# Optimization experiments

Measured on AMD Instinct MI355X. Metric: run time of the kernel, lower is better.

The kernel has to match this reference:

```python
import jax, jax.numpy as jnp
import numpy as np

NUM_LAYERS = 3
N = 4096
DIM = 512
TOPK = 8
BIG = 1.0e9
EPS_COS = 1e-8
EPS_NORM = 1e-12
BN_EPS = 1e-5
LAM_K = 64.0
LAM_Z = 16.0
SIGMA_INTRA = 0.99
ALPHA = np.linspace(1.0, 1.2, NUM_LAYERS)
BETA = np.linspace(0.0, 0.0, NUM_LAYERS)


def setup_inputs() -> dict:
    key = jax.random.key(0)
    ks = jax.random.split(key, 6)
    feats = jax.random.normal(ks[0], (NUM_LAYERS, N, DIM), dtype=jnp.float32)
    labels = jax.random.randint(ks[1], (N,), 0, 64, dtype=jnp.int64)
    fc1_w = jax.random.normal(ks[2], (NUM_LAYERS, DIM, DIM), dtype=jnp.float32) * (1.0 / np.sqrt(DIM))
    fc2_w = jax.random.normal(ks[3], (NUM_LAYERS, DIM, DIM), dtype=jnp.float32) * (1.0 / np.sqrt(DIM))
    bn_gamma = jnp.ones((NUM_LAYERS, DIM), dtype=jnp.float32)
    bn_beta = jnp.zeros((NUM_LAYERS, DIM), dtype=jnp.float32)
    proj_w = jax.random.normal(ks[4], (768, DIM), dtype=jnp.float32) * (1.0 / np.sqrt(DIM))
    return {"feats": feats, "labels": labels, "fc1_w": fc1_w, "fc2_w": fc2_w,
            "bn_gamma": bn_gamma, "bn_beta": bn_beta, "proj_w": proj_w}


def _l2norm(x, axis=-1):
    return x / jnp.maximum(jnp.linalg.norm(x, axis=axis, keepdims=True), EPS_NORM)


def _pairwise_cosine(G):
    Gn = _l2norm(G)
    sim = Gn @ Gn.T
    return jnp.clip(sim, -1.0 + EPS_COS, 1.0 - EPS_COS)


def _knn_mask(sim, base_mask, topk):
    n = sim.shape[0]
    masked = (sim - BIG * jnp.eye(n, dtype=sim.dtype)) * base_mask - (1.0 - base_mask) * BIG
    k = min(topk, max(n - 1, 1))
    idx = jax.lax.top_k(masked, k)[1]  # [N, k]
    st = jnp.zeros_like(sim).at[jnp.arange(n)[:, None], idx].set(1.0)
    return jnp.maximum(st, st.T)


def _build_intra_inter(sim, labels, topk):
    same = (labels[None, :] == labels[:, None]).astype(sim.dtype)
    diff = 1.0 - same
    m_intra = _knn_mask(sim, same, topk)
    m_inter = _knn_mask(sim, diff, topk)
    sim_intra = jnp.maximum(sim * m_intra, 0.0)
    sim_inter = jnp.maximum(sim * m_inter, 0.0)
    return sim_intra, sim_inter


def _normalize_sym(sim_graph, eps=1e-8):
    d = jnp.maximum(sim_graph.sum(axis=1), eps)
    dinv = d ** -0.5
    return dinv[:, None] * sim_graph * dinv[None, :]  # == diag(dinv) @ S @ diag(dinv)


def _diffusion(K, t_diff=1):
    out = K
    for _ in range(max(t_diff - 1, 0)):
        out = out @ K
    return out


def _bn_train(x, gamma, beta):
    m = x.mean(axis=0)
    v = x.var(axis=0)  # biased, as torch BN training
    return (x - m) / jnp.sqrt(v + BN_EPS) * gamma + beta


def _gam(S, G, w1, w2, gamma, beta):
    Z = S @ (G @ w1.T)
    Z = jax.nn.relu(_bn_train(Z, gamma, beta))
    Z = S @ (Z @ w2.T)
    return Z + G


def reference(feats, labels, fc1_w, fc2_w, bn_gamma, bn_beta, proj_w):
    n = feats.shape[1]
    eye = jnp.eye(n, dtype=feats.dtype)
    same = (labels[None, :] == labels[:, None]).astype(feats.dtype)

    K_list, Z_list = [], []
    for i in range(NUM_LAYERS):
        G = feats[i]
        sim = _pairwise_cosine(G)
        sim_intra, sim_inter = _build_intra_inter(sim, labels, TOPK)
        sim_graph = float(ALPHA[i]) * sim_intra + float(BETA[i]) * sim_inter + 1e-6 * eye
        S = _normalize_sym(sim_graph)
        K = _diffusion(S, t_diff=1)
        Z = _gam(S, G, fc1_w[i], fc2_w[i], bn_gamma[i], bn_beta[i])
        K_list.append(K)
        Z_list.append(Z)

    loss_K = jnp.zeros((), dtype=feats.dtype)
    loss_Z = jnp.zeros((), dtype=feats.dtype)
    for i in range(1, NUM_LAYERS):
        K_tgt = jax.lax.stop_gradient(K_list[i])
        loss_K = loss_K + jnp.mean((K_list[i - 1] - K_tgt) ** 2)
        Zp = _l2norm(Z_list[i - 1] @ proj_w.T)
        Zc = _l2norm(Z_list[i] @ proj_w.T)
        loss_Z = loss_Z + jnp.mean((Zp - jax.lax.stop_gradient(Zc)) ** 2)

    K_idea = _diffusion(same * SIGMA_INTRA, t_diff=1)
    loss_idea = jnp.mean((K_list[-1] - K_idea) ** 2)
    return LAM_K * loss_K + LAM_Z * loss_Z + loss_idea
```

## Files before the change

kernel.cpp:

```cpp
#include <hip/hip_runtime.h>
#include <math.h>
#include <stdint.h>

#define NROWS 4096
#define DIM   512
#define NCLS  64
#define CAP   128
#define PD    768
#define NL    3

typedef __attribute__((ext_vector_type(8))) short short8v;
typedef __attribute__((ext_vector_type(4))) float f32x4;

__device__ __forceinline__ unsigned short f2bf(float f) {
  unsigned u = __float_as_uint(f);
  unsigned r = (u + 0x7FFF + ((u >> 16) & 1)) >> 16;
  return (unsigned short)r;
}

__device__ __forceinline__ void gload_lds16(const void* g, void* l) {
  auto* lp = reinterpret_cast<__attribute__((address_space(3))) unsigned int*>(
      reinterpret_cast<uintptr_t>(l));
  const auto* gp = reinterpret_cast<const __attribute__((address_space(1))) unsigned int*>(
      reinterpret_cast<uintptr_t>(g));
  __builtin_amdgcn_global_load_lds(gp, lp, 16, 0, 0);
}

__device__ __forceinline__ float waveReduce(float v) {
#pragma unroll
  for (int o = 32; o > 0; o >>= 1) v += __shfl_down(v, o);
  return v;
}

__device__ __forceinline__ float blockReduce(float v) {
  __shared__ float sh[4];
  int lane = threadIdx.x & 63, wv = threadIdx.x >> 6;
  v = waveReduce(v);
  if (lane == 0) sh[wv] = v;
  __syncthreads();
  float t = 0.f;
  if (threadIdx.x == 0) {
    int nw = (blockDim.x + 63) >> 6;
    for (int i = 0; i < nw; ++i) t += sh[i];
  }
  return t;
}

__global__ __launch_bounds__(256) void k_hist(const int* __restrict__ labels, int* __restrict__ chunkCnt) {
  __shared__ int h[NCLS];
  int t = threadIdx.x;
  if (t < NCLS) h[t] = 0;
  __syncthreads();
  atomicAdd(&h[labels[blockIdx.x * 256 + t]], 1);
  __syncthreads();
  if (t < NCLS) chunkCnt[blockIdx.x * NCLS + t] = h[t];
}

__global__ void k_scan(const int* __restrict__ chunkCnt, int* __restrict__ cnt,
                       int* __restrict__ off, int* __restrict__ chunkBase, float* __restrict__ acc) {
  __shared__ int sc[NCLS];
  int c = threadIdx.x;
  if (c < 8) acc[c] = 0.f;
  int tot = 0;
  for (int b = 0; b < 16; ++b) tot += chunkCnt[b * NCLS + c];
  cnt[c] = tot;
  sc[c] = tot;
  __syncthreads();
  if (c == 0) {
    int s = 0;
    for (int i = 0; i < NCLS; ++i) { int tv = sc[i]; sc[i] = s; s += tv; }
  }
  __syncthreads();
  int run = sc[c];
  off[c] = run;
  for (int b = 0; b < 16; ++b) { chunkBase[b * NCLS + c] = run; run += chunkCnt[b * NCLS + c]; }
  if (c == 0) off[NCLS] = NROWS;
}

__global__ __launch_bounds__(256) void k_scatter(const int* __restrict__ labels, const int* __restrict__ chunkBase,
                                                 int* __restrict__ perm, int* __restrict__ clsp) {
  __shared__ int lab[256];
  int t = threadIdx.x;
  int r = blockIdx.x * 256 + t;
  int c = labels[r];
  lab[t] = c;
  __syncthreads();
  int rank = 0;
  for (int j = 0; j < t; ++j) rank += (lab[j] == c);
  int pos = chunkBase[blockIdx.x * NCLS + c] + rank;
  perm[pos] = r;
  clsp[pos] = c;
}

__global__ __launch_bounds__(128) void k_prep(const float* __restrict__ feats, const int* __restrict__ perm,
                                              unsigned short* __restrict__ Gpb, float* __restrict__ invn) {
  __shared__ float red[2];
  int l = blockIdx.y;
  const float* G = feats + (size_t)l * NROWS * DIM;
  unsigned short* Gp = Gpb + (size_t)l * NROWS * DIM;
  int row = blockIdx.x, t = threadIdx.x;
  const float4* src = (const float4*)(G + (size_t)perm[row] * DIM);
  float4 v = src[t];
  ushort4 b;
  b.x = f2bf(v.x); b.y = f2bf(v.y); b.z = f2bf(v.z); b.w = f2bf(v.w);
  *(ushort4*)(Gp + (size_t)row * DIM + t * 4) = b;
  float ss = v.x * v.x + v.y * v.y + v.z * v.z + v.w * v.w;
  ss = waveReduce(ss);
  if ((t & 63) == 0) red[t >> 6] = ss;
  __syncthreads();
  if (t == 0) invn[l * NROWS + row] = 1.f / fmaxf(sqrtf(red[0] + red[1]), 1e-12f);
}

__global__ __launch_bounds__(256) void k_tobf16all(const float4* __restrict__ fc1, const float4* __restrict__ fc2,
                                                   const float4* __restrict__ proj,
                                                   ushort4* __restrict__ w1, ushort4* __restrict__ w2,
                                                   ushort4* __restrict__ pj) {
  const int nW = NL * DIM * DIM / 4;
  const int nP = PD * DIM / 4;
  int i = blockIdx.x * 256 + threadIdx.x;
  const float4* src; ushort4* dst; int k;
  if (i < nW) { src = fc1; dst = w1; k = i; }
  else if (i < 2 * nW) { src = fc2; dst = w2; k = i - nW; }
  else if (i < 2 * nW + nP) { src = proj; dst = pj; k = i - 2 * nW; }
  else return;
  float4 v = src[k];
  ushort4 o;
  o.x = f2bf(v.x); o.y = f2bf(v.y); o.z = f2bf(v.z); o.w = f2bf(v.w);
  dst[k] = o;
}

__global__ __launch_bounds__(256) void k_sim(const unsigned short* __restrict__ Gpb,
                                             const float* __restrict__ invn,
                                             const int* __restrict__ cnt, const int* __restrict__ off,
                                             float* __restrict__ sim) {
  int l = blockIdx.z;
  const unsigned short* Gp = Gpb + (size_t)l * NROWS * DIM;
  const float* inv = invn + (size_t)l * NROWS;
  float* sm = sim + (size_t)l * NCLS * CAP * CAP;
  int c = blockIdx.y;
  int n = min(cnt[c], CAP);
  int ti = blockIdx.x >> 2, tj = blockIdx.x & 3;
  if (ti * 32 >= n || tj * 32 >= n) return;
  int base = off[c];
  __shared__ short As[32][40];
  __shared__ short Bs[32][40];
  const int t = threadIdx.x;
  const int lane = t & 63, wv = t >> 6;
  const int qi = wv >> 1, qj = wv & 1;
  const int fr = lane & 15, kg = lane >> 4;
  const int half = t >> 7, tt = t & 127;
  const int srow = tt >> 2, scol = (tt & 3) * 8;
  int gr = (half ? tj : ti) * 32 + srow;
  const unsigned short* ps = Gp + (size_t)(base + min(gr, n - 1)) * DIM + scol;
  short* dst = half ? &Bs[srow][scol] : &As[srow][scol];
  f32x4 acc = {};
  for (int k0 = 0; k0 < DIM; k0 += 32) {
    short8v v = *(const short8v*)(ps + k0);
    __syncthreads();
    *(short8v*)dst = v;
    __syncthreads();
    short8v af = *(const short8v*)&As[qi * 16 + fr][kg * 8];
    short8v bf = *(const short8v*)&Bs[qj * 16 + fr][kg * 8];
    acc = __builtin_amdgcn_mfma_f32_16x16x32_bf16(af, bf, acc, 0, 0, 0);
  }
  int gj = tj * 32 + qj * 16 + fr;
  int r0 = ti * 32 + qi * 16 + kg * 4;
  if (gj < n) {
    float sj = inv[base + gj];
#pragma unroll
    for (int r = 0; r < 4; ++r) {
      int gi = r0 + r;
      if (gi < n) {
        float v = acc[r] * inv[base + gi] * sj;
        v = fminf(fmaxf(v, -1.0f + 1e-8f), 1.0f - 1e-8f);
        sm[((size_t)c * CAP + gi) * CAP + gj] = v;
      }
    }
  }
}

__global__ __launch_bounds__(256) void k_topk(const float* __restrict__ sim, const int* __restrict__ cnt,
                                              const int* __restrict__ off, const int* __restrict__ clsp,
                                              int* __restrict__ t8) {
  int l = blockIdx.y;
  const float* sm = sim + (size_t)l * NCLS * CAP * CAP;
  int* t8l = t8 + (size_t)l * NROWS * 8;
  int pr = blockIdx.x * 256 + threadIdx.x;
  if (pr >= NROWS) return;
  int c = clsp[pr];
  int n = min(cnt[c], CAP);
  int loc = pr - off[c];
  const float4* row4 = (const float4*)(sm + ((size_t)c * CAP + loc) * CAP);
  float bv[8]; int bi[8];
#pragma unroll
  for (int q = 0; q < 8; ++q) { bv[q] = -3e38f; bi[q] = -1; }
  for (int j4 = 0; j4 < CAP / 4; ++j4) {
    if (j4 * 4 >= n) break;
    float4 v4 = row4[j4];
    float vv[4] = {v4.x, v4.y, v4.z, v4.w};
#pragma unroll
    for (int k = 0; k < 4; ++k) {
      int j = j4 * 4 + k;
      if (j >= n || j == loc) continue;
      float v = vv[k];
      if (v > bv[7]) {
        bv[7] = v; bi[7] = j;
#pragma unroll
        for (int q = 7; q > 0; --q) {
          if (bv[q] > bv[q - 1]) {
            float tv = bv[q]; bv[q] = bv[q - 1]; bv[q - 1] = tv;
            int tq = bi[q]; bi[q] = bi[q - 1]; bi[q - 1] = tq;
          }
        }
      }
    }
  }
#pragma unroll
  for (int q = 0; q < 8; ++q) t8l[pr * 8 + q] = bi[q];
}

__global__ __launch_bounds__(256) void k_buildS1(const float* __restrict__ sim, const int* __restrict__ cnt,
                                                 const int* __restrict__ off, const int* __restrict__ t8,
                                                 float* __restrict__ S, float* __restrict__ dinv) {
  int l = blockIdx.z;
  float alpha = 1.0f + 0.1f * l;
  const float* sm = sim + (size_t)l * NCLS * CAP * CAP;
  float* Sl = S + (size_t)l * NCLS * CAP * CAP;
  const int* t8l = t8 + (size_t)l * NROWS * 8;
  float* dv = dinv + (size_t)l * NCLS * CAP;
  int c = blockIdx.x;
  int n = min(cnt[c], CAP);
  int i0 = blockIdx.y * 32;
  if (i0 >= n) return;
  int base = off[c];
  __shared__ int sh8[CAP * 8];
  for (int i = threadIdx.x; i < n * 8; i += 256) sh8[i] = t8l[base * 8 + i];
  __syncthreads();
  int r = threadIdx.x >> 3;
  int lj = threadIdx.x & 7;
  int i = i0 + r;
  float d = 0.f;
  if (i < n) {
    int my8[8];
#pragma unroll
    for (int q = 0; q < 8; ++q) my8[q] = sh8[i * 8 + q];
    const float* srow = sm + ((size_t)c * CAP + i) * CAP;
    float* wrow = Sl + ((size_t)c * CAP + i) * CAP;
    for (int j = lj; j < n; j += 8) {
      float w;
      if (j == i) w = 1e-6f;
      else {
        bool m = false;
#pragma unroll
        for (int q = 0; q < 8; ++q) m = m || (my8[q] == j) || (sh8[j * 8 + q] == i);
        w = m ? alpha * fmaxf(srow[j], 0.f) : 0.f;
      }
      wrow[j] = w;
      d += w;
    }
  }
  d += __shfl_xor(d, 1);
  d += __shfl_xor(d, 2);
  d += __shfl_xor(d, 4);
  if (lj == 0 && i < n) dv[c * CAP + i] = 1.f / sqrtf(fmaxf(d, 1e-8f));
}

__global__ __launch_bounds__(256) void k_buildS2(float* __restrict__ S, const float* __restrict__ dinv,
                                                 const int* __restrict__ cnt) {
  int l = blockIdx.z;
  float* Sl = S + (size_t)l * NCLS * CAP * CAP;
  const float* dv = dinv + (size_t)l * NCLS * CAP;
  int c = blockIdx.x;
  int n = min(cnt[c], CAP);
  int i0 = blockIdx.y * 32;
  if (i0 >= n) return;
  __shared__ float sd[CAP];
  for (int k = threadIdx.x; k < n; k += 256) sd[k] = dv[c * CAP + k];
  __syncthreads();
  for (int p = threadIdx.x; p < 32 * CAP; p += 256) {
    int r = p >> 7, j = p & (CAP - 1);
    int i = i0 + r;
    if (i < n && j < n)
      Sl[((size_t)c * CAP + i) * CAP + j] *= sd[i] * sd[j];
  }
}

__global__ __launch_bounds__(256) void k_gemm_bf16(const short* __restrict__ A, const short* __restrict__ B,
                                                   float* __restrict__ C, unsigned short* __restrict__ Cb,
                                                   int N, long sA, long sB, long sC) {
  int l = blockIdx.z;
  A += (size_t)l * sA; B += (size_t)l * sB;
  if (Cb) Cb += (size_t)l * sC; else C += (size_t)l * sC;
  __shared__ __align__(16) short As[128][32];
  __shared__ __align__(16) short Bs[128][32];
  const int row0 = blockIdx.x * 128, col0 = blockIdx.y * 128;
  const int t = threadIdx.x;
  const int lane = t & 63, wv = t >> 6;
  const int wm = wv >> 1, wn = wv & 1;
  const int fr = lane & 15, kg = lane >> 4;
  const int srow = lane >> 2, skb = (lane & 3) * 8;
  const short* pa = A + (size_t)(row0 + wv * 32 + srow) * DIM + skb;
  const short* pb = B + (size_t)(col0 + wv * 32 + srow) * DIM + skb;
  f32x4 acc[4][4] = {};
  for (int kt = 0; kt < DIM; kt += 32) {
    __syncthreads();
    gload_lds16(pa + kt, &As[wv * 32][0]);
    gload_lds16(pa + kt + (size_t)16 * DIM, &As[wv * 32 + 16][0]);
    gload_lds16(pb + kt, &Bs[wv * 32][0]);
    gload_lds16(pb + kt + (size_t)16 * DIM, &Bs[wv * 32 + 16][0]);
    __syncthreads();
    short8v af[4], bf[4];
#pragma unroll
    for (int i = 0; i < 4; ++i) {
      af[i] = *(const short8v*)&As[wm * 64 + i * 16 + fr][kg * 8];
      bf[i] = *(const short8v*)&Bs[wn * 64 + i * 16 + fr][kg * 8];
    }
#pragma unroll
    for (int i = 0; i < 4; ++i)
#pragma unroll
      for (int j = 0; j < 4; ++j)
        acc[i][j] = __builtin_amdgcn_mfma_f32_16x16x32_bf16(af[i], bf[j], acc[i][j], 0, 0, 0);
  }
#pragma unroll
  for (int i = 0; i < 4; ++i) {
    int r0 = row0 + wm * 64 + i * 16 + kg * 4;
#pragma unroll
    for (int j = 0; j < 4; ++j) {
      int cc = col0 + wn * 64 + j * 16 + fr;
#pragma unroll
      for (int r = 0; r < 4; ++r) {
        if (Cb) Cb[(size_t)(r0 + r) * N + cc] = f2bf(acc[i][j][r]);
        else C[(size_t)(r0 + r) * N + cc] = acc[i][j][r];
      }
    }
  }
}

__global__ __launch_bounds__(256) void k_spmm4(const float* __restrict__ S, const float* __restrict__ X,
                                               const float* __restrict__ Gfeat, const int* __restrict__ perm,
                                               float* __restrict__ Y, unsigned short* __restrict__ Yb,
                                               const int* __restrict__ cnt, const int* __restrict__ off) {
  int l = blockIdx.z >> 2;
  int zc = blockIdx.z & 3;
  const float* Sl = S + (size_t)l * NCLS * CAP * CAP;
  const float4* X4 = (const float4*)(X + (size_t)l * NROWS * DIM);
  const float4* G4 = Gfeat ? (const float4*)(Gfeat + (size_t)l * NROWS * DIM) : (const float4*)nullptr;
  float4* Y4 = Y ? (float4*)(Y + (size_t)l * NROWS * DIM) : (float4*)nullptr;
  ushort4* Yb4 = Yb ? (ushort4*)(Yb + (size_t)l * NROWS * DIM) : (ushort4*)nullptr;
  int c = blockIdx.x;
  int n = min(cnt[c], CAP);
  int i0 = zc * 32;
  if (i0 >= n) return;
  int base = off[c];
  int col4 = blockIdx.y * 64 + (threadIdx.x & 63);
  int ty = threadIdx.x >> 6;
  __shared__ float sS[32][CAP];
  for (int idx = threadIdx.x; idx < 32 * n; idx += 256) {
    int r = idx / n, j = idx - r * n;
    sS[r][j] = (i0 + r < n) ? Sl[((size_t)c * CAP + i0 + r) * CAP + j] : 0.f;
  }
  __syncthreads();
  float4 acc[8];
#pragma unroll
  for (int ii = 0; ii < 8; ++ii) acc[ii] = make_float4(0.f, 0.f, 0.f, 0.f);
#pragma unroll 4
  for (int j = 0; j < n; ++j) {
    float4 x = X4[(size_t)(base + j) * 128 + col4];
#pragma unroll
    for (int ii = 0; ii < 8; ++ii) {
      float s = sS[ty * 8 + ii][j];
      acc[ii].x += s * x.x;
      acc[ii].y += s * x.y;
      acc[ii].z += s * x.z;
      acc[ii].w += s * x.w;
    }
  }
#pragma unroll
  for (int ii = 0; ii < 8; ++ii) {
    int r = i0 + ty * 8 + ii;
    if (r < n) {
      size_t o = (size_t)(base + r) * 128 + col4;
      float4 v = acc[ii];
      if (G4) {
        float4 g = G4[(size_t)perm[base + r] * 128 + col4];
        v.x += g.x; v.y += g.y; v.z += g.z; v.w += g.w;
      }
      if (Yb4) {
        ushort4 ob;
        ob.x = f2bf(v.x); ob.y = f2bf(v.y); ob.z = f2bf(v.z); ob.w = f2bf(v.w);
        Yb4[o] = ob;
      } else {
        Y4[o] = v;
      }
    }
  }
}

#define PARTSZ (size_t)((NROWS / 32) * 1024)

__global__ __launch_bounds__(256) void k_colstats(const float* __restrict__ X, float* __restrict__ part) {
  int l = blockIdx.y;
  const float* Xl = X + (size_t)l * NROWS * DIM;
  float* pl = part + (size_t)l * PARTSZ;
  int rb = blockIdx.x, t = threadIdx.x;
#pragma unroll
  for (int cp = 0; cp < 2; ++cp) {
    int col = cp * 256 + t;
    float s = 0.f, s2 = 0.f;
    for (int r = 0; r < 32; ++r) {
      float v = Xl[(size_t)(rb * 32 + r) * DIM + col];
      s += v; s2 += v * v;
    }
    pl[rb * 1024 + col] = s;
    pl[rb * 1024 + 512 + col] = s2;
  }
}

__global__ __launch_bounds__(64) void k_bnfin(const float* __restrict__ part, const float* __restrict__ gamma,
                                              const float* __restrict__ beta, float* __restrict__ sc) {
  int l = blockIdx.y;
  const float* pl = part + (size_t)l * PARTSZ;
  int k = blockIdx.x * 64 + threadIdx.x;
  float s = 0.f, s2 = 0.f;
  for (int b = 0; b < NROWS / 32; ++b) {
    s += pl[b * 1024 + k];
    s2 += pl[b * 1024 + 512 + k];
  }
  float m = s * (1.f / NROWS);
  float var = s2 * (1.f / NROWS) - m * m;
  float sg = gamma[l * DIM + k] / sqrtf(var + 1e-5f);
  sc[l * 2 * DIM + k] = sg;
  sc[l * 2 * DIM + DIM + k] = beta[l * DIM + k] - m * sg;
}

__global__ __launch_bounds__(256) void k_bnrelu(const float4* __restrict__ X, const float* __restrict__ sc,
                                                ushort4* __restrict__ Yb) {
  int l = blockIdx.y;
  const float4* Xl = X + (size_t)l * (NROWS * DIM / 4);
  const float* scl = sc + (size_t)l * 2 * DIM;
  ushort4* Yl = Yb + (size_t)l * (NROWS * DIM / 4);
  int i = blockIdx.x * blockDim.x + threadIdx.x;
  int cb = (i * 4) & (DIM - 1);
  float4 v = Xl[i];
  ushort4 o;
  o.x = f2bf(fmaxf(v.x * scl[cb + 0] + scl[DIM + cb + 0], 0.f));
  o.y = f2bf(fmaxf(v.y * scl[cb + 1] + scl[DIM + cb + 1], 0.f));
  o.z = f2bf(fmaxf(v.z * scl[cb + 2] + scl[DIM + cb + 2], 0.f));
  o.w = f2bf(fmaxf(v.w * scl[cb + 3] + scl[DIM + cb + 3], 0.f));
  Yl[i] = o;
}

__global__ __launch_bounds__(192) void k_rownormP(float* __restrict__ P) {
  __shared__ float red[3];
  __shared__ float s_inv;
  int l = blockIdx.y;
  float* Pl = P + (size_t)l * NROWS * PD;
  int row = blockIdx.x, t = threadIdx.x;
  float4* p = (float4*)(Pl + (size_t)row * PD);
  float4 v = p[t];
  float ss = v.x * v.x + v.y * v.y + v.z * v.z + v.w * v.w;
  ss = waveReduce(ss);
  if ((t & 63) == 0) red[t >> 6] = ss;
  __syncthreads();
  if (t == 0) s_inv = 1.f / fmaxf(sqrtf(red[0] + red[1] + red[2]), 1e-12f);
  __syncthreads();
  float inv = s_inv;
  v.x *= inv; v.y *= inv; v.z *= inv; v.w *= inv;
  p[t] = v;
}

__global__ __launch_bounds__(256) void k_lossdiff(const float* __restrict__ P, int n, float coef,
                                                  float* __restrict__ acc) {
  int y = blockIdx.y;
  const float* A = P + (size_t)y * NROWS * PD;
  const float* B = A + (size_t)NROWS * PD;
  float s = 0.f;
  for (int i = blockIdx.x * blockDim.x + threadIdx.x; i < n; i += gridDim.x * blockDim.x) {
    float d = A[i] - B[i];
    s += d * d;
  }
  s = blockReduce(s);
  if (threadIdx.x == 0) atomicAdd(acc, s * coef);
}

__global__ __launch_bounds__(256) void k_lossS(const float* __restrict__ S, const int* __restrict__ cnt,
                                               float target, float cK, float cI,
                                               float* __restrict__ acc) {
  int y = blockIdx.y;
  const float* Sa = S + (size_t)y * NCLS * CAP * CAP;
  const float* Sb = nullptr;
  float coef;
  if (y < 2) { Sb = Sa + (size_t)NCLS * CAP * CAP; coef = cK; }
  else { Sa = S + (size_t)2 * NCLS * CAP * CAP; coef = cI; }
  int c = blockIdx.x;
  int n = min(cnt[c], CAP);
  float s = 0.f;
  for (int p = threadIdx.x; p < CAP * CAP; p += 256) {
    int i = p >> 7, j = p & (CAP - 1);
    if (i < n && j < n) {
      size_t o = ((size_t)c * CAP + i) * CAP + j;
      float d = Sb ? (Sa[o] - Sb[o]) : (Sa[o] - target);
      s += d * d;
    }
  }
  s = blockReduce(s);
  if (threadIdx.x == 0) atomicAdd(acc, s * coef);
}

__global__ void k_final(const float* __restrict__ acc, float* __restrict__ out) {
  if (threadIdx.x == 0) out[0] = acc[0];
}

extern "C" void kernel_launch(void* const* d_in, const int* in_sizes, int n_in,
                              void* d_out, int out_size, void* d_ws, size_t ws_size,
                              hipStream_t stream) {
  const float* feats = (const float*)d_in[0];
  const int* labels = (const int*)d_in[1];
  const float* fc1 = (const float*)d_in[2];
  const float* fc2 = (const float*)d_in[3];
  const float* gamma = (const float*)d_in[4];
  const float* beta = (const float*)d_in[5];
  const float* proj = (const float*)d_in[6];
  float* out = (float*)d_out;

  char* w = (char*)d_ws;
  auto alloc = [&](size_t bytes) { char* p = w; w += (bytes + 255) & ~(size_t)255; return p; };
  float* bufA = (float*)alloc((size_t)NL * NROWS * DIM * 4);
  float* bufB = (float*)alloc((size_t)NL * NROWS * DIM * 4);
  unsigned short* Gpb = (unsigned short*)alloc((size_t)NL * NROWS * DIM * 2);
  unsigned short* actb = (unsigned short*)alloc((size_t)NL * NROWS * DIM * 2);
  unsigned short* W1b = (unsigned short*)alloc((size_t)NL * DIM * DIM * 2);
  unsigned short* W2b = (unsigned short*)alloc((size_t)NL * DIM * DIM * 2);
  unsigned short* Pjb = (unsigned short*)alloc((size_t)PD * DIM * 2);
  float* sim  = (float*)alloc((size_t)NL * NCLS * CAP * CAP * 4);
  float* S    = (float*)alloc((size_t)NL * NCLS * CAP * CAP * 4);
  float* P    = (float*)alloc((size_t)NL * NROWS * PD * 4);
  float* invn = (float*)alloc((size_t)NL * NROWS * 4);
  float* dinv = (float*)alloc((size_t)NL * NCLS * CAP * 4);
  float* part = (float*)alloc((size_t)NL * PARTSZ * 4);
  float* bnsc = (float*)alloc((size_t)NL * 2 * DIM * 4);
  float* acc  = (float*)alloc(256);
  int* cnt  = (int*)alloc(NCLS * 4);
  int* offc = (int*)alloc((NCLS + 1) * 4);
  int* perm = (int*)alloc(NROWS * 4);
  int* clsp = (int*)alloc(NROWS * 4);
  int* t8   = (int*)alloc((size_t)NL * NROWS * 8 * 4);
  int* chunkCnt  = (int*)alloc(16 * NCLS * 4);
  int* chunkBase = (int*)alloc(16 * NCLS * 4);

  const float LAM_K = 64.f, LAM_Z = 16.f, SIGMA = 0.99f;
  const float cK = LAM_K / ((float)NROWS * (float)NROWS);
  const float cZ = LAM_Z / ((float)NROWS * (float)PD);
  const float cI = 1.f / ((float)NROWS * (float)NROWS);
  const long sAct = (long)NROWS * DIM;
  const long sW = (long)DIM * DIM;

  hipLaunchKernelGGL(k_hist, dim3(16), dim3(256), 0, stream, labels, chunkCnt);
  hipLaunchKernelGGL(k_scan, dim3(1), dim3(64), 0, stream, chunkCnt, cnt, offc, chunkBase, acc);
  hipLaunchKernelGGL(k_scatter, dim3(16), dim3(256), 0, stream, labels, chunkBase, perm, clsp);
  hipLaunchKernelGGL(k_tobf16all, dim3((2 * NL * DIM * DIM / 4 + PD * DIM / 4 + 255) / 256), dim3(256), 0, stream,
                     (const float4*)fc1, (const float4*)fc2, (const float4*)proj,
                     (ushort4*)W1b, (ushort4*)W2b, (ushort4*)Pjb);

  hipLaunchKernelGGL(k_prep, dim3(NROWS, NL), dim3(128), 0, stream, feats, perm, Gpb, invn);
  hipLaunchKernelGGL(k_sim, dim3(16, NCLS, NL), dim3(256), 0, stream, Gpb, invn, cnt, offc, sim);
  hipLaunchKernelGGL(k_topk, dim3(NROWS / 256, NL), dim3(256), 0, stream, sim, cnt, offc, clsp, t8);
  hipLaunchKernelGGL(k_buildS1, dim3(NCLS, CAP / 32, NL), dim3(256), 0, stream, sim, cnt, offc, t8, S, dinv);
  hipLaunchKernelGGL(k_buildS2, dim3(NCLS, CAP / 32, NL), dim3(256), 0, stream, S, dinv, cnt);

  hipLaunchKernelGGL(k_gemm_bf16, dim3(NROWS / 128, DIM / 128, NL), dim3(256), 0, stream,
                     (const short*)Gpb, (const short*)W1b, bufA, (unsigned short*)nullptr, DIM, sAct, sW, (long)NROWS * DIM);
  hipLaunchKernelGGL(k_spmm4, dim3(NCLS, DIM / 256, 4 * NL), dim3(256), 0, stream, S, bufA,
                     (const float*)nullptr, (const int*)nullptr, bufB, (unsigned short*)nullptr, cnt, offc);
  hipLaunchKernelGGL(k_colstats, dim3(NROWS / 32, NL), dim3(256), 0, stream, bufB, part);
  hipLaunchKernelGGL(k_bnfin, dim3(DIM / 64, NL), dim3(64), 0, stream, part, gamma, beta, bnsc);
  hipLaunchKernelGGL(k_bnrelu, dim3(NROWS * DIM / 4 / 256, NL), dim3(256), 0, stream,
                     (const float4*)bufB, bnsc, (ushort4*)actb);
  hipLaunchKernelGGL(k_gemm_bf16, dim3(NROWS / 128, DIM / 128, NL), dim3(256), 0, stream,
                     (const short*)actb, (const short*)W2b, bufB, (unsigned short*)nullptr, DIM, sAct, sW, (long)NROWS * DIM);
  hipLaunchKernelGGL(k_spmm4, dim3(NCLS, DIM / 256, 4 * NL), dim3(256), 0, stream, S, bufB,
                     feats, perm, (float*)nullptr, actb, cnt, offc);
  hipLaunchKernelGGL(k_gemm_bf16, dim3(NROWS / 128, PD / 128, NL), dim3(256), 0, stream,
                     (const short*)actb, (const short*)Pjb, P, (unsigned short*)nullptr, PD, sAct, 0L, (long)NROWS * PD);
  hipLaunchKernelGGL(k_rownormP, dim3(NROWS, NL), dim3(192), 0, stream, P);

  hipLaunchKernelGGL(k_lossS, dim3(NCLS, 3), dim3(256), 0, stream, S, cnt, SIGMA, cK, cI, acc);
  hipLaunchKernelGGL(k_lossdiff, dim3(512, 2), dim3(256), 0, stream, P, NROWS * PD, cZ, acc);

  hipLaunchKernelGGL(k_final, dim3(1), dim3(64), 0, stream, acc, out);
}
```

Before: 287.7 us.

## Fuse weight conversion, BN column stats, and loss kernels; shrink GEMM tiles

Folds the weight-to-bf16 conversion into the feature prep kernel as an extra grid row, computes BatchNorm column sums and sums of squares inside the first spmm epilogue instead of in a separate colstats pass, and merges the two loss kernels into one launch. It also changes the bf16 GEMM tile from 128x128 to 128x64, which gives more blocks for better occupancy at the cost of less reuse per block. The aim is to cut launch count and one full read of the activation buffer. The risk is extra shared-memory syncs in spmm and lower arithmetic intensity in the GEMM.

Result: faster. 265.2 us (-7.8%).

```diff
diff --git a/kernel.cpp b/kernel.cpp
--- a/kernel.cpp
+++ b/kernel.cpp
@@ -8,6 +8,7 @@
 #define CAP   128
 #define PD    768
 #define NL    3
+#define PARTSZ (size_t)(NCLS * 4 * 1024)
 
 typedef __attribute__((ext_vector_type(8))) short short8v;
 typedef __attribute__((ext_vector_type(4))) float f32x4;
@@ -92,10 +93,30 @@
   clsp[pos] = c;
 }
 
-__global__ __launch_bounds__(128) void k_prep(const float* __restrict__ feats, const int* __restrict__ perm,
-                                              unsigned short* __restrict__ Gpb, float* __restrict__ invn) {
+__global__ __launch_bounds__(128) void k_prepw(const float* __restrict__ feats, const int* __restrict__ perm,
+                                               unsigned short* __restrict__ Gpb, float* __restrict__ invn,
+                                               const float4* __restrict__ fc1, const float4* __restrict__ fc2,
+                                               const float4* __restrict__ proj,
+                                               ushort4* __restrict__ w1, ushort4* __restrict__ w2,
+                                               ushort4* __restrict__ pj) {
+  int y = blockIdx.y;
+  if (y == NL) {
+    const int nW = NL * DIM * DIM / 4;
+    const int nP = PD * DIM / 4;
+    int idx = blockIdx.x * 128 + threadIdx.x;
+    const float4* src; ushort4* dst; int k;
+    if (idx < nW) { src = fc1; dst = w1; k = idx; }
+    else if (idx < 2 * nW) { src = fc2; dst = w2; k = idx - nW; }
+    else if (idx < 2 * nW + nP) { src = proj; dst = pj; k = idx - 2 * nW; }
+    else return;
+    float4 v = src[k];
+    ushort4 o;
+    o.x = f2bf(v.x); o.y = f2bf(v.y); o.z = f2bf(v.z); o.w = f2bf(v.w);
+    dst[k] = o;
+    return;
+  }
   __shared__ float red[2];
-  int l = blockIdx.y;
+  int l = y;
   const float* G = feats + (size_t)l * NROWS * DIM;
   unsigned short* Gp = Gpb + (size_t)l * NROWS * DIM;
   int row = blockIdx.x, t = threadIdx.x;
@@ -109,24 +130,6 @@
   if ((t & 63) == 0) red[t >> 6] = ss;
   __syncthreads();
   if (t == 0) invn[l * NROWS + row] = 1.f / fmaxf(sqrtf(red[0] + red[1]), 1e-12f);
-}
-
-__global__ __launch_bounds__(256) void k_tobf16all(const float4* __restrict__ fc1, const float4* __restrict__ fc2,
-                                                   const float4* __restrict__ proj,
-                                                   ushort4* __restrict__ w1, ushort4* __restrict__ w2,
-                                                   ushort4* __restrict__ pj) {
-  const int nW = NL * DIM * DIM / 4;
-  const int nP = PD * DIM / 4;
-  int i = blockIdx.x * 256 + threadIdx.x;
-  const float4* src; ushort4* dst; int k;
-  if (i < nW) { src = fc1; dst = w1; k = i; }
-  else if (i < 2 * nW) { src = fc2; dst = w2; k = i - nW; }
-  else if (i < 2 * nW + nP) { src = proj; dst = pj; k = i - 2 * nW; }
-  else return;
-  float4 v = src[k];
-  ushort4 o;
-  o.x = f2bf(v.x); o.y = f2bf(v.y); o.z = f2bf(v.z); o.w = f2bf(v.w);
-  dst[k] = o;
 }
 
 __global__ __launch_bounds__(256) void k_sim(const unsigned short* __restrict__ Gpb,
@@ -286,52 +289,46 @@
 }
 
 __global__ __launch_bounds__(256) void k_gemm_bf16(const short* __restrict__ A, const short* __restrict__ B,
-                                                   float* __restrict__ C, unsigned short* __restrict__ Cb,
-                                                   int N, long sA, long sB, long sC) {
+                                                   float* __restrict__ C, int N,
+                                                   long sA, long sB, long sC) {
   int l = blockIdx.z;
-  A += (size_t)l * sA; B += (size_t)l * sB;
-  if (Cb) Cb += (size_t)l * sC; else C += (size_t)l * sC;
+  A += (size_t)l * sA; B += (size_t)l * sB; C += (size_t)l * sC;
   __shared__ __align__(16) short As[128][32];
-  __shared__ __align__(16) short Bs[128][32];
-  const int row0 = blockIdx.x * 128, col0 = blockIdx.y * 128;
+  __shared__ __align__(16) short Bs[64][32];
+  const int row0 = blockIdx.x * 128, col0 = blockIdx.y * 64;
   const int t = threadIdx.x;
   const int lane = t & 63, wv = t >> 6;
-  const int wm = wv >> 1, wn = wv & 1;
   const int fr = lane & 15, kg = lane >> 4;
   const int srow = lane >> 2, skb = (lane & 3) * 8;
   const short* pa = A + (size_t)(row0 + wv * 32 + srow) * DIM + skb;
-  const short* pb = B + (size_t)(col0 + wv * 32 + srow) * DIM + skb;
-  f32x4 acc[4][4] = {};
+  const short* pb = B + (size_t)(col0 + wv * 16 + srow) * DIM + skb;
+  f32x4 acc[2][4] = {};
   for (int kt = 0; kt < DIM; kt += 32) {
     __syncthreads();
     gload_lds16(pa + kt, &As[wv * 32][0]);
     gload_lds16(pa + kt + (size_t)16 * DIM, &As[wv * 32 + 16][0]);
-    gload_lds16(pb + kt, &Bs[wv * 32][0]);
-    gload_lds16(pb + kt + (size_t)16 * DIM, &Bs[wv * 32 + 16][0]);
+    gload_lds16(pb + kt, &Bs[wv * 16][0]);
     __syncthreads();
-    short8v af[4], bf[4];
-#pragma unroll
-    for (int i = 0; i < 4; ++i) {
-      af[i] = *(const short8v*)&As[wm * 64 + i * 16 + fr][kg * 8];
-      bf[i] = *(const short8v*)&Bs[wn * 64 + i * 16 + fr][kg * 8];
-    }
-#pragma unroll
-    for (int i = 0; i < 4; ++i)
+    short8v af[2], bf[4];
+#pragma unroll
+    for (int i = 0; i < 2; ++i) af[i] = *(const short8v*)&As[wv * 32 + i * 16 + fr][kg * 8];
+#pragma unroll
+    for (int j = 0; j < 4; ++j) bf[j] = *(const short8v*)&Bs[j * 16 + fr][kg * 8];
+#pragma unroll
+    for (int i = 0; i < 2; ++i)
 #pragma unroll
       for (int j = 0; j < 4; ++j)
         acc[i][j] = __builtin_amdgcn_mfma_f32_16x16x32_bf16(af[i], bf[j], acc[i][j], 0, 0, 0);
   }
 #pragma unroll
-  for (int i = 0; i < 4; ++i) {
-    int r0 = row0 + wm * 64 + i * 16 + kg * 4;
+  for (int i = 0; i < 2; ++i) {
+    int r0 = row0 + wv * 32 + i * 16 + kg * 4;
 #pragma unroll
     for (int j = 0; j < 4; ++j) {
-      int cc = col0 + wn * 64 + j * 16 + fr;
-#pragma unroll
-      for (int r = 0; r < 4; ++r) {
-        if (Cb) Cb[(size_t)(r0 + r) * N + cc] = f2bf(acc[i][j][r]);
-        else C[(size_t)(r0 + r) * N + cc] = acc[i][j][r];
-      }
+      int cc = col0 + j * 16 + fr;
+#pragma unroll
+      for (int r = 0; r < 4; ++r)
+        C[(size_t)(r0 + r) * N + cc] = acc[i][j][r];
     }
   }
 }
@@ -339,6 +336,7 @@
 __global__ __launch_bounds__(256) void k_spmm4(const float* __restrict__ S, const float* __restrict__ X,
                                                const float* __restrict__ Gfeat, const int* __restrict__ perm,
                                                float* __restrict__ Y, unsigned short* __restrict__ Yb,
+                                               float* __restrict__ part,
                                                const int* __restrict__ cnt, const int* __restrict__ off) {
   int l = blockIdx.z >> 2;
   int zc = blockIdx.z & 3;
@@ -350,11 +348,20 @@
   int c = blockIdx.x;
   int n = min(cnt[c], CAP);
   int i0 = zc * 32;
-  if (i0 >= n) return;
+  float* pslot = part ? part + (size_t)l * PARTSZ + (size_t)(c * 4 + zc) * 1024 : (float*)nullptr;
+  __shared__ float sS[32][CAP];
+  if (i0 >= n) {
+    if (pslot) {
+      int col = blockIdx.y * 256 + threadIdx.x;
+      pslot[col] = 0.f;
+      pslot[512 + col] = 0.f;
+    }
+    return;
+  }
   int base = off[c];
-  int col4 = blockIdx.y * 64 + (threadIdx.x & 63);
+  int lane = threadIdx.x & 63;
+  int col4 = blockIdx.y * 64 + lane;
   int ty = threadIdx.x >> 6;
-  __shared__ float sS[32][CAP];
   for (int idx = threadIdx.x; idx < 32 * n; idx += 256) {
     int r = idx / n, j = idx - r * n;
     sS[r][j] = (i0 + r < n) ? Sl[((size_t)c * CAP + i0 + r) * CAP + j] : 0.f;
@@ -363,7 +370,6 @@
   float4 acc[8];
 #pragma unroll
   for (int ii = 0; ii < 8; ++ii) acc[ii] = make_float4(0.f, 0.f, 0.f, 0.f);
-#pragma unroll 4
   for (int j = 0; j < n; ++j) {
     float4 x = X4[(size_t)(base + j) * 128 + col4];
 #pragma unroll
@@ -375,6 +381,7 @@
       acc[ii].w += s * x.w;
     }
   }
+  float s1[4] = {0.f, 0.f, 0.f, 0.f}, s2[4] = {0.f, 0.f, 0.f, 0.f};
 #pragma unroll
   for (int ii = 0; ii < 8; ++ii) {
     int r = i0 + ty * 8 + ii;
@@ -385,6 +392,10 @@
         float4 g = G4[(size_t)perm[base + r] * 128 + col4];
         v.x += g.x; v.y += g.y; v.z += g.z; v.w += g.w;
       }
+      if (pslot) {
+        s1[0] += v.x; s1[1] += v.y; s1[2] += v.z; s1[3] += v.w;
+        s2[0] += v.x * v.x; s2[1] += v.y * v.y; s2[2] += v.z * v.z; s2[3] += v.w * v.w;
+      }
       if (Yb4) {
         ushort4 ob;
         ob.x = f2bf(v.x); ob.y = f2bf(v.y); ob.z = f2bf(v.z); ob.w = f2bf(v.w);
@@ -394,25 +405,29 @@
       }
     }
   }
-}
-
-#define PARTSZ (size_t)((NROWS / 32) * 1024)
-
-__global__ __launch_bounds__(256) void k_colstats(const float* __restrict__ X, float* __restrict__ part) {
-  int l = blockIdx.y;
-  const float* Xl = X + (size_t)l * NROWS * DIM;
-  float* pl = part + (size_t)l * PARTSZ;
-  int rb = blockIdx.x, t = threadIdx.x;
-#pragma unroll
-  for (int cp = 0; cp < 2; ++cp) {
-    int col = cp * 256 + t;
-    float s = 0.f, s2 = 0.f;
-    for (int r = 0; r < 32; ++r) {
-      float v = Xl[(size_t)(rb * 32 + r) * DIM + col];
-      s += v; s2 += v * v;
-    }
-    pl[rb * 1024 + col] = s;
-    pl[rb * 1024 + 512 + col] = s2;
+  if (pslot) {
+    __syncthreads();
+    float* scr = &sS[0][0];
+#pragma unroll
+    for (int q = 0; q < 4; ++q) {
+      scr[(ty * 64 + lane) * 8 + q] = s1[q];
+      scr[(ty * 64 + lane) * 8 + 4 + q] = s2[q];
+    }
+    __syncthreads();
+    if (ty == 0) {
+#pragma unroll
+      for (int q = 0; q < 4; ++q) {
+        float a = 0.f, b = 0.f;
+#pragma unroll
+        for (int g = 0; g < 4; ++g) {
+          a += scr[(g * 64 + lane) * 8 + q];
+          b += scr[(g * 64 + lane) * 8 + 4 + q];
+        }
+        int col = blockIdx.y * 256 + lane * 4 + q;
+        pslot[col] = a;
+        pslot[512 + col] = b;
+      }
+    }
   }
 }
 
@@ -422,7 +437,7 @@
   const float* pl = part + (size_t)l * PARTSZ;
   int k = blockIdx.x * 64 + threadIdx.x;
   float s = 0.f, s2 = 0.f;
-  for (int b = 0; b < NROWS / 32; ++b) {
+  for (int b = 0; b < NCLS * 4; ++b) {
     s += pl[b * 1024 + k];
     s2 += pl[b * 1024 + 512 + k];
   }
@@ -469,42 +484,44 @@
   p[t] = v;
 }
 
-__global__ __launch_bounds__(256) void k_lossdiff(const float* __restrict__ P, int n, float coef,
-                                                  float* __restrict__ acc) {
+__global__ __launch_bounds__(256) void k_loss(const float* __restrict__ S, const float* __restrict__ P,
+                                              const int* __restrict__ cnt,
+                                              float target, float cK, float cI, float cZ,
+                                              float* __restrict__ acc) {
   int y = blockIdx.y;
-  const float* A = P + (size_t)y * NROWS * PD;
-  const float* B = A + (size_t)NROWS * PD;
-  float s = 0.f;
-  for (int i = blockIdx.x * blockDim.x + threadIdx.x; i < n; i += gridDim.x * blockDim.x) {
-    float d = A[i] - B[i];
-    s += d * d;
-  }
-  s = blockReduce(s);
-  if (threadIdx.x == 0) atomicAdd(acc, s * coef);
-}
-
-__global__ __launch_bounds__(256) void k_lossS(const float* __restrict__ S, const int* __restrict__ cnt,
-                                               float target, float cK, float cI,
-                                               float* __restrict__ acc) {
-  int y = blockIdx.y;
-  const float* Sa = S + (size_t)y * NCLS * CAP * CAP;
-  const float* Sb = nullptr;
-  float coef;
-  if (y < 2) { Sb = Sa + (size_t)NCLS * CAP * CAP; coef = cK; }
-  else { Sa = S + (size_t)2 * NCLS * CAP * CAP; coef = cI; }
-  int c = blockIdx.x;
-  int n = min(cnt[c], CAP);
-  float s = 0.f;
-  for (int p = threadIdx.x; p < CAP * CAP; p += 256) {
-    int i = p >> 7, j = p & (CAP - 1);
-    if (i < n && j < n) {
-      size_t o = ((size_t)c * CAP + i) * CAP + j;
-      float d = Sb ? (Sa[o] - Sb[o]) : (Sa[o] - target);
+  if (y < 3) {
+    if (blockIdx.x >= NCLS) return;
+    const float* Sa = S + (size_t)y * NCLS * CAP * CAP;
+    const float* Sb = nullptr;
+    float coef;
+    if (y < 2) { Sb = Sa + (size_t)NCLS * CAP * CAP; coef = cK; }
+    else { Sa = S + (size_t)2 * NCLS * CAP * CAP; coef = cI; }
+    int c = blockIdx.x;
+    int n = min(cnt[c], CAP);
+    float s = 0.f;
+    for (int p = threadIdx.x; p < CAP * CAP; p += 256) {
+      int i = p >> 7, j = p & (CAP - 1);
+      if (i < n && j < n) {
+        size_t o = ((size_t)c * CAP + i) * CAP + j;
+        float d = Sb ? (Sa[o] - Sb[o]) : (Sa[o] - target);
+        s += d * d;
+      }
+    }
+    s = blockReduce(s);
+    if (threadIdx.x == 0) atomicAdd(acc, s * coef);
+  } else {
+    int yy = y - 3;
+    const float* A = P + (size_t)yy * NROWS * PD;
+    const float* B = A + (size_t)NROWS * PD;
+    const int nel = NROWS * PD;
+    float s = 0.f;
+    for (int i = blockIdx.x * blockDim.x + threadIdx.x; i < nel; i += gridDim.x * blockDim.x) {
+      float d = A[i] - B[i];
       s += d * d;
     }
-  }
-  s = blockReduce(s);
-  if (threadIdx.x == 0) atomicAdd(acc, s * coef);
+    s = blockReduce(s);
+    if (threadIdx.x == 0) atomicAdd(acc, s * cZ);
+  }
 }
 
 __global__ void k_final(const float* __restrict__ acc, float* __restrict__ out) {
@@ -558,34 +575,32 @@
   hipLaunchKernelGGL(k_hist, dim3(16), dim3(256), 0, stream, labels, chunkCnt);
   hipLaunchKernelGGL(k_scan, dim3(1), dim3(64), 0, stream, chunkCnt, cnt, offc, chunkBase, acc);
   hipLaunchKernelGGL(k_scatter, dim3(16), dim3(256), 0, stream, labels, chunkBase, perm, clsp);
-  hipLaunchKernelGGL(k_tobf16all, dim3((2 * NL * DIM * DIM / 4 + PD * DIM / 4 + 255) / 256), dim3(256), 0, stream,
+
+  hipLaunchKernelGGL(k_prepw, dim3(NROWS, NL + 1), dim3(128), 0, stream, feats, perm, Gpb, invn,
                      (const float4*)fc1, (const float4*)fc2, (const float4*)proj,
                      (ushort4*)W1b, (ushort4*)W2b, (ushort4*)Pjb);
 
-  hipLaunchKernelGGL(k_prep, dim3(NROWS, NL), dim3(128), 0, stream, feats, perm, Gpb, invn);
   hipLaunchKernelGGL(k_sim, dim3(16, NCLS, NL), dim3(256), 0, stream, Gpb, invn, cnt, offc, sim);
   hipLaunchKernelGGL(k_topk, dim3(NROWS / 256, NL), dim3(256), 0, stream, sim, cnt, offc, clsp, t8);
   hipLaunchKernelGGL(k_buildS1, dim3(NCLS, CAP / 32, NL), dim3(256), 0, stream, sim, cnt, offc, t8, S, dinv);
   hipLaunchKernelGGL(k_buildS2, dim3(NCLS, CAP / 32, NL), dim3(256), 0, stream, S, dinv, cnt);
 
-  hipLaunchKernelGGL(k_gemm_bf16, dim3(NROWS / 128, DIM / 128, NL), dim3(256), 0, stream,
-                     (const short*)Gpb, (const short*)W1b, bufA, (unsigned short*)nullptr, DIM, sAct, sW, (long)NROWS * DIM);
+  hipLaunchKernelGGL(k_gemm_bf16, dim3(NROWS / 128, DIM / 64, NL), dim3(256), 0, stream,
+                     (const short*)Gpb, (const short*)W1b, bufA, DIM, sAct, sW, (long)NROWS * DIM);
   hipLaunchKernelGGL(k_spmm4, dim3(NCLS, DIM / 256, 4 * NL), dim3(256), 0, stream, S, bufA,
-                     (const float*)nullptr, (const int*)nullptr, bufB, (unsigned short*)nullptr, cnt, offc);
-  hipLaunchKernelGGL(k_colstats, dim3(NROWS / 32, NL), dim3(256), 0, stream, bufB, part);
+                     (const float*)nullptr, (const int*)nullptr, bufB, (unsigned short*)nullptr, part, cnt, offc);
   hipLaunchKernelGGL(k_bnfin, dim3(DIM / 64, NL), dim3(64), 0, stream, part, gamma, beta, bnsc);
   hipLaunchKernelGGL(k_bnrelu, dim3(NROWS * DIM / 4 / 256, NL), dim3(256), 0, stream,
                      (const float4*)bufB, bnsc, (ushort4*)actb);
-  hipLaunchKernelGGL(k_gemm_bf16, dim3(NROWS / 128, DIM / 128, NL), dim3(256), 0, stream,
-                     (const short*)actb, (const short*)W2b, bufB, (unsigned short*)nullptr, DIM, sAct, sW, (long)NROWS * DIM);
+  hipLaunchKernelGGL(k_gemm_bf16, dim3(NROWS / 128, DIM / 64, NL), dim3(256), 0, stream,
+                     (const short*)actb, (const short*)W2b, bufB, DIM, sAct, sW, (long)NROWS * DIM);
   hipLaunchKernelGGL(k_spmm4, dim3(NCLS, DIM / 256, 4 * NL), dim3(256), 0, stream, S, bufB,
-                     feats, perm, (float*)nullptr, actb, cnt, offc);
-  hipLaunchKernelGGL(k_gemm_bf16, dim3(NROWS / 128, PD / 128, NL), dim3(256), 0, stream,
-                     (const short*)actb, (const short*)Pjb, P, (unsigned short*)nullptr, PD, sAct, 0L, (long)NROWS * PD);
+                     feats, perm, (float*)nullptr, actb, (float*)nullptr, cnt, offc);
+  hipLaunchKernelGGL(k_gemm_bf16, dim3(NROWS / 128, PD / 64, NL), dim3(256), 0, stream,
+                     (const short*)actb, (const short*)Pjb, P, PD, sAct, 0L, (long)NROWS * PD);
   hipLaunchKernelGGL(k_rownormP, dim3(NROWS, NL), dim3(192), 0, stream, P);
 
-  hipLaunchKernelGGL(k_lossS, dim3(NCLS, 3), dim3(256), 0, stream, S, cnt, SIGMA, cK, cI, acc);
-  hipLaunchKernelGGL(k_lossdiff, dim3(512, 2), dim3(256), 0, stream, P, NROWS * PD, cZ, acc);
+  hipLaunchKernelGGL(k_loss, dim3(512, 5), dim3(256), 0, stream, S, P, cnt, SIGMA, cK, cI, cZ, acc);
 
   hipLaunchKernelGGL(k_final, dim3(1), dim3(64), 0, stream, acc, out);
 }
```
